# Performance work log

Hardware: AMD Instinct MI355X
Metric: run time of the kernel (lower is better)

The kernel has to match this reference:

```python
import jax, jax.numpy as jnp
import numpy as np

HEADS = 8
DIM_HEAD = 32


def setup_inputs() -> dict:
    key = jax.random.key(0)
    ks = jax.random.split(key, 10)
    B, N, D = 64, 256, 256            # B = b_true * tie_dim = 1 * 64
    INNER = HEADS * DIM_HEAD          # 256
    x = jax.random.normal(ks[0], (B, N, D), dtype=jnp.float32)
    mask = jax.random.randint(ks[1], (B, N), 0, 2).astype(bool)
    attn_bias = jax.random.normal(ks[2], (1, HEADS, N, N), dtype=jnp.float32)
    # Note: original init zeros to_out/gating weights; we use random params
    # (scaled) so the baseline output is non-trivial for correctness testing.
    s = 0.05
    Wq = jax.random.normal(ks[3], (D, INNER), dtype=jnp.float32) * s
    Wkv = jax.random.normal(ks[4], (D, 2 * INNER), dtype=jnp.float32) * s
    Wg = jax.random.normal(ks[5], (D, INNER), dtype=jnp.float32) * s
    bg = jax.random.normal(ks[6], (INNER,), dtype=jnp.float32) * s
    Wo = jax.random.normal(ks[7], (INNER, D), dtype=jnp.float32) * s
    bo = jax.random.normal(ks[8], (D,), dtype=jnp.float32) * s
    return {"x": x, "mask": mask, "attn_bias": attn_bias, "Wq": Wq,
            "Wkv": Wkv, "Wg": Wg, "bg": bg, "Wo": Wo, "bo": bo,
            "tie_dim": 64}


def reference(x, mask, attn_bias, Wq, Wkv, Wg, bg, Wo, bo, tie_dim):
    B, N, D = x.shape
    h, dh = HEADS, DIM_HEAD
    scale = dh ** -0.5

    # projections (self-attention: context = x)
    q = (x @ Wq).reshape(B, N, h, dh).transpose(0, 2, 1, 3) * scale  # b h n d
    k, v = jnp.split(x @ Wkv, 2, axis=-1)
    k = k.reshape(B, N, h, dh).transpose(0, 2, 1, 3)                 # b h n d
    v = v.reshape(B, N, h, dh).transpose(0, 2, 1, 3)                 # b h n d

    # tie_dim: average q over the r (MSA row) dim, keep per-row k
    r = tie_dim
    b = B // r
    q_tied = q.reshape(b, r, h, N, dh).mean(axis=1)                  # b h i d
    k_r = k.reshape(b, r, h, N, dh)                                  # b r h j d
    dots = jnp.einsum('bhid,brhjd->brhij', q_tied, k_r)
    dots = dots.reshape(B, h, N, N)                                  # (b r) h i j

    dots = dots + attn_bias

    # mask: pairwise row/col mask (context_mask == mask for self-attn)
    pair_mask = mask[:, None, :, None] & mask[:, None, None, :]      # B 1 i j
    mask_value = -jnp.finfo(dots.dtype).max
    dots = jnp.where(pair_mask, dots, mask_value)

    attn = jax.nn.softmax(dots, axis=-1)
    out = jnp.einsum('bhij,bhjd->bhid', attn, v)
    out = out.transpose(0, 2, 1, 3).reshape(B, N, h * dh)            # b n (h d)

    gates = jax.nn.sigmoid(x @ Wg + bg)
    out = out * gates
    return out @ Wo + bo
```

## Files before the change

### kernel.cpp

```cpp
#include <hip/hip_runtime.h>
#include <math.h>

typedef unsigned short ushort_t;
typedef unsigned int uint_t;
typedef __attribute__((ext_vector_type(8))) short short8v;
typedef __attribute__((ext_vector_type(4))) float f32x4;

#define NEG_MAX (-3.402823466e+38f)

#define OFF_KH    0
#define OFF_VP    4194304
#define OFF_GATES 6291456
#define OFF_XHI   8388608
#define OFF_ATTHI OFF_XHI
#define OFF_BTHI  12582912
#define OFF_BTLO  12713984
#define OFF_QTH   12845056
#define OFF_BIASP 12976128
#define OFF_MASK  13500416

__device__ __forceinline__ ushort_t f2bf(float x) {
    uint_t u = __float_as_uint(x);
    u = (u + 0x7fffu + ((u >> 16) & 1u)) >> 16;
    return (ushort_t)u;
}
__device__ __forceinline__ float bf2f(ushort_t u) {
    return __uint_as_float(((uint_t)u) << 16);
}
__device__ __forceinline__ void gl2lds16(const void* g, void* l) {
    typedef const __attribute__((address_space(1))) uint32_t* gptr_t;
    typedef __attribute__((address_space(3))) uint32_t* lptr_t;
    __builtin_amdgcn_global_load_lds((gptr_t)(uintptr_t)g,
                                     (lptr_t)(uintptr_t)l, 16, 0, 0);
}

__global__ __launch_bounds__(256) void prep_kernel(
    const float* __restrict__ x, const unsigned char* __restrict__ mraw,
    const float* __restrict__ bias, const float* __restrict__ Wkv,
    const float* __restrict__ Wg, const float* __restrict__ Wo,
    const float* __restrict__ Wq,
    ushort_t* __restrict__ xhi,
    uint_t* __restrict__ maskb,
    ushort_t* __restrict__ bthi, ushort_t* __restrict__ btlo,
    float* __restrict__ biasP, ushort_t* __restrict__ qPh) {
    __shared__ int cnt[256];
    __shared__ float xrow[256];
    const int bid = blockIdx.x, t = threadIdx.x;
    if (bid < 1) {
        int c = 0;
        for (int i = t; i < 4096; i += 256)
            if ((i & 3) != 0 && mraw[i] != 0) c++;
        cnt[t] = c;
        __syncthreads();
        for (int s = 128; s > 0; s >>= 1) {
            if (t < s) cnt[t] += cnt[t + s];
            __syncthreads();
        }
        int isBool = cnt[0] > 16;
        const int* mi32 = (const int*)mraw;
#pragma unroll
        for (int wq = 0; wq < 2; wq++) {
            int widx = t * 2 + wq;
            int j0 = widx * 32;
            uint_t wordv = 0;
            if (isBool) {
                for (int k = 0; k < 32; k++)
                    wordv |= (mraw[j0 + k] ? 1u : 0u) << k;
            } else {
                for (int k = 0; k < 32; k++)
                    wordv |= (mi32[j0 + k] ? 1u : 0u) << k;
            }
            maskb[widx] = wordv;
        }
    } else if (bid < 1025) {
        int idx = (bid - 1) * 256 + t;
        int n = idx >> 8, k = idx & 255;
        float v;
        if (n < 512)      v = Wkv[(size_t)k * 512 + n];
        else if (n < 768) v = Wg[(size_t)k * 256 + (n - 512)];
        else              v = Wo[(size_t)k * 256 + (n - 768)];
        ushort_t h = f2bf(v);
        bthi[idx] = h;
        btlo[idx] = f2bf(v - bf2f(h));
    } else if (bid < 1537) {
        int idx = (bid - 1025) * 256 + t;
        int lane = idx & 63, g2 = idx >> 6;
        int mf = g2 & 3, nf = (g2 >> 2) & 1, jt = (g2 >> 3) & 3;
        int iq = (g2 >> 5) & 7, h = g2 >> 8;
        int lr = lane & 15, lg = lane >> 4;
        float4 v = *(const float4*)(bias +
            (size_t)(h * 256 + iq * 32 + nf * 16 + lr) * 256 +
            jt * 64 + mf * 16 + lg * 4);
        *(float4*)(biasP + (size_t)idx * 4) = v;
    } else {
        int i = bid - 1537;
        float ssum = 0.f;
#pragma unroll 8
        for (int b8 = 0; b8 < 64; b8++) {
            size_t idx = (size_t)(b8 * 256 + i) * 256 + t;
            float v = x[idx];
            xhi[idx] = f2bf(v);
            ssum += v;
        }
        xrow[t] = ssum * (1.0f / 64.0f);
        __syncthreads();
        float s = 0.f;
        for (int k = 0; k < 256; k++)
            s = fmaf(xrow[k], Wq[(size_t)k * 256 + t], s);
        s *= 0.17677669529663687f;
        int h = t >> 5, d = t & 31, lg = d >> 3, e = d & 7;
        int g = i >> 4, lr = i & 15;
        int a = (((h * 16 + g) * 4 + lg) * 16 + lr) * 8 + e;
        qPh[a] = f2bf(s);
    }
}

template <int EPI, int MT, int NT, int TERMS>
__global__ __launch_bounds__(256) void mfma_gemm(
    const ushort_t* __restrict__ Ahi, const ushort_t* __restrict__ Alo,
    const ushort_t* __restrict__ Bthi, const ushort_t* __restrict__ Btlo,
    const float* __restrict__ bias, float* __restrict__ C,
    ushort_t* __restrict__ kh, ushort_t* __restrict__ vP,
    ushort_t* __restrict__ gatesP, int gridn) {
    constexpr int BM = MT * 32, BN = NT * 32;
    constexpr int ASZ = BM * 32 * 2;
    constexpr int BSZ = BN * 32 * 2;
    constexpr bool HAS_AL = (TERMS == 2 || TERMS == 3);
    constexpr bool HAS_BL = (TERMS == 3 || TERMS == 4);
    constexpr int AL_OFF = 2 * ASZ;
    constexpr int BH_OFF = AL_OFF + (HAS_AL ? 2 * ASZ : 0);
    constexpr int BL_OFF = BH_OFF + 2 * BSZ;
    constexpr int SMEM_BYTES = BL_OFF + (HAS_BL ? 2 * BSZ : 0);
    __shared__ __align__(16) char smem[SMEM_BYTES];
    char* aH = smem;
    char* aL = smem + AL_OFF;
    char* bH = smem + BH_OFF;
    char* bL = smem + BL_OFF;

    const int t = threadIdx.x;
    const int nwg = gridDim.x, cpx = nwg >> 3;
    const int bid = blockIdx.x;
    const int sid = (bid & 7) * cpx + (bid >> 3);
    const int m0 = (sid / gridn) * BM;
    const int n0 = (sid % gridn) * BN;
    const int wid = t >> 6, lane = t & 63;
    const int wr = wid >> 1, wc = wid & 1;
    const int lr = lane & 15, lg = lane >> 4;

    auto STAGE = [&](int d, int ks) {
        const int k0 = ks * 32;
#pragma unroll
        for (int it = 0; it < BM / 64; ++it) {
            int c = t + it * 256;
            int row = c >> 2, sub = c & 3;
            size_t ga = (size_t)(m0 + row) * 256 + k0 + sub * 8;
            gl2lds16(Ahi + ga, aH + d * ASZ + c * 16);
            if constexpr (HAS_AL)
                gl2lds16(Alo + ga, aL + d * ASZ + c * 16);
        }
#pragma unroll
        for (int it = 0; it < BN / 64; ++it) {
            int c = t + it * 256;
            int row = c >> 2, sub = c & 3;
            size_t gb = (size_t)(n0 + row) * 256 + k0 + sub * 8;
            gl2lds16(Bthi + gb, bH + d * BSZ + c * 16);
            if constexpr (HAS_BL)
                gl2lds16(Btlo + gb, bL + d * BSZ + c * 16);
        }
    };

    f32x4 acc[MT][NT] = {};

    STAGE(0, 0);
    asm volatile("s_waitcnt vmcnt(0)" ::: "memory");
    __syncthreads();

    int cur = 0;
    for (int ks = 0; ks < 8; ++ks) {
        if (ks < 7) STAGE(cur ^ 1, ks + 1);

        const ushort_t* Ap = (const ushort_t*)(aH + cur * ASZ);
        const ushort_t* ALp = (const ushort_t*)(aL + cur * ASZ);
        const ushort_t* Bp = (const ushort_t*)(bH + cur * BSZ);
        const ushort_t* BLp = (const ushort_t*)(bL + cur * BSZ);

        short8v ah[MT], al[MT], bh[NT], bl[NT];
#pragma unroll
        for (int m = 0; m < MT; m++) {
            int off = (wr * (MT * 16) + m * 16 + lr) * 32 + lg * 8;
            ah[m] = *(const short8v*)&Ap[off];
            if constexpr (HAS_AL) al[m] = *(const short8v*)&ALp[off];
        }
#pragma unroll
        for (int n = 0; n < NT; n++) {
            int off = (wc * (NT * 16) + n * 16 + lr) * 32 + lg * 8;
            bh[n] = *(const short8v*)&Bp[off];
            if constexpr (HAS_BL) bl[n] = *(const short8v*)&BLp[off];
        }
#pragma unroll
        for (int m = 0; m < MT; m++)
#pragma unroll
            for (int n = 0; n < NT; n++) {
                acc[m][n] = __builtin_amdgcn_mfma_f32_16x16x32_bf16(
                    ah[m], bh[n], acc[m][n], 0, 0, 0);
                if constexpr (HAS_AL)
                    acc[m][n] = __builtin_amdgcn_mfma_f32_16x16x32_bf16(
                        al[m], bh[n], acc[m][n], 0, 0, 0);
                if constexpr (HAS_BL)
                    acc[m][n] = __builtin_amdgcn_mfma_f32_16x16x32_bf16(
                        ah[m], bl[n], acc[m][n], 0, 0, 0);
            }

        if (ks < 7) {
            asm volatile("s_waitcnt vmcnt(0)" ::: "memory");
            __syncthreads();
        }
        cur ^= 1;
    }

#pragma unroll
    for (int m = 0; m < MT; m++)
#pragma unroll
        for (int n = 0; n < NT; n++) {
            int gr0 = m0 + wr * (MT * 16) + m * 16 + lg * 4;
            int gc = n0 + wc * (NT * 16) + n * 16 + lr;
            if (EPI == 0) {
                if (gc < 256) {
                    int hh_ = gc >> 5, dk = gc & 31;
                    int lgk = dk >> 3, ek = dk & 7;
#pragma unroll
                    for (int r = 0; r < 4; r++) {
                        int gr = gr0 + r;
                        int bb = gr >> 8, j = gr & 255;
                        int jt = j >> 6, mfk = (j >> 4) & 3, lrk = j & 15;
                        size_t a =
                            (((((size_t)(bb * 8 + hh_) * 4 + jt) * 4 + mfk) * 4
                              + lgk) * 16 + lrk) * 8 + ek;
                        kh[a] = f2bf(acc[m][n][r]);
                    }
                } else if (gc < 512) {
                    int cc = gc - 256;
                    int hh_ = cc >> 5, dv = cc & 31;
                    int mfv = dv >> 4, lrv = dv & 15;
                    int gr = gr0;
                    int bb = gr >> 8, j = gr & 255;
                    int jt = j >> 6, hbv = (j >> 5) & 1;
                    int lgv = (j >> 3) & 3, ev = j & 7;
                    size_t a =
                        ((((((size_t)(bb * 8 + hh_) * 4 + jt) * 2 + hbv) * 2
                           + mfv) * 4 + lgv) * 16 + lrv) * 8 + ev;
                    ushort4 hv;
                    hv.x = f2bf(acc[m][n][0]);
                    hv.y = f2bf(acc[m][n][1]);
                    hv.z = f2bf(acc[m][n][2]);
                    hv.w = f2bf(acc[m][n][3]);
                    *(ushort4*)(vP + a) = hv;
                } else {
                    int c = gc - 512;
                    int hh_ = c >> 5, d = c & 31;
                    int mdv = d >> 4, lga = (d >> 2) & 3, ev = d & 3;
#pragma unroll
                    for (int r = 0; r < 4; r++) {
                        int gr = gr0 + r;
                        int bb = gr >> 8, i = gr & 255;
                        int i16 = i >> 4, lra = i & 15;
                        size_t a =
                            ((((size_t)(bb * 8 + hh_) * 16 + i16) * 2 + mdv)
                             * 64 + lga * 16 + lra) * 4 + ev;
                        float v = acc[m][n][r];
                        float g = 1.f / (1.f + __expf(-(v + bias[gc - 512])));
                        gatesP[a] = f2bf(g);
                    }
                }
            } else {
#pragma unroll
                for (int r = 0; r < 4; r++)
                    C[(size_t)(gr0 + r) * 256 + gc] = acc[m][n][r] + bias[gc];
            }
        }
}

__global__ __launch_bounds__(256) void attn_mfma_kernel(
    const ushort_t* __restrict__ qPh, const ushort_t* __restrict__ kh,
    const ushort_t* __restrict__ vP, const ushort_t* __restrict__ gatesP,
    const float* __restrict__ biasP, const uint_t* __restrict__ maskb,
    ushort_t* __restrict__ atthi) {
    __shared__ __align__(16) ushort_t Pb[4][16 * 88];
    const int bid = blockIdx.x;
    const int sid = ((bid & 7) << 8) | (bid >> 3);
    const int b = sid >> 5;
    const int h = (sid >> 2) & 7;
    const int qq = sid & 3;
    const int t = threadIdx.x;
    const int w = t >> 6, lane = t & 63;
    const int lr = lane & 15, lg = lane >> 4;
    const int i0 = qq * 64 + w * 16;
    const int i16 = qq * 4 + w;
    ushort_t* pbh = Pb[w];

    uint_t mw[8];
#pragma unroll
    for (int k = 0; k < 8; k++) mw[k] = maskb[b * 8 + k];
    const uint_t mi = (mw[i0 >> 5] >> ((i0 & 31) + lr)) & 1u;

    short8v qf;
    {
        size_t off = ((((size_t)h * 16 + i16) * 4 + lg) * 16 + lr) * 8;
        qf = *(const short8v*)(qPh + off);
    }
    uint2 gva, gvb;
    {
        size_t ga = ((((size_t)(b * 8 + h) * 16 + i16) * 2 + 0) * 64 + lane) * 4;
        gva = *(const uint2*)(gatesP + ga);
        gvb = *(const uint2*)(gatesP + ga + 256);
    }

    const float* bbase = biasP +
        (size_t)(h * 256 + (i16 >> 1) * 32 + (i16 & 1) * 4) * 256 +
        (size_t)lane * 4;

    float m_run = NEG_MAX, l_run = 0.f;
    f32x4 acc_o[2] = {};

    short8v kf[2][4];
    float4 bf[2][4];
    short8v vf[2][2][2];
#pragma unroll
    for (int mf = 0; mf < 4; mf++) {
        size_t off = ((((size_t)(b * 8 + h) * 4 + 0) * 4 + mf) * 4 + lg);
        kf[0][mf] = *(const short8v*)(kh + (off * 16 + lr) * 8);
        bf[0][mf] = *(const float4*)(bbase + (size_t)mf * 256);
    }
#pragma unroll
    for (int hb = 0; hb < 2; hb++)
#pragma unroll
        for (int mv = 0; mv < 2; mv++) {
            size_t off = ((((((size_t)(b * 8 + h) * 4 + 0) * 2 + hb) * 2
                           + mv) * 4 + lg) * 16 + lr) * 8;
            vf[0][hb][mv] = *(const short8v*)(vP + off);
        }

#pragma unroll
    for (int jt = 0; jt < 4; ++jt) {
        const int cur = jt & 1, nxt = cur ^ 1;
        if (jt < 3) {
#pragma unroll
            for (int mf = 0; mf < 4; mf++) {
                size_t off = ((((size_t)(b * 8 + h) * 4 + (jt + 1)) * 4 + mf)
                              * 4 + lg);
                kf[nxt][mf] = *(const short8v*)(kh + (off * 16 + lr) * 8);
                bf[nxt][mf] = *(const float4*)(bbase +
                                               (size_t)((jt + 1) * 8 + mf) * 256);
            }
#pragma unroll
            for (int hb = 0; hb < 2; hb++)
#pragma unroll
                for (int mv = 0; mv < 2; mv++) {
                    size_t off = ((((((size_t)(b * 8 + h) * 4 + (jt + 1)) * 2
                                    + hb) * 2 + mv) * 4 + lg) * 16 + lr) * 8;
                    vf[nxt][hb][mv] = *(const short8v*)(vP + off);
                }
        }

        f32x4 s[4];
        __builtin_amdgcn_s_setprio(1);
#pragma unroll
        for (int mf = 0; mf < 4; mf++) {
            f32x4 a = {};
            s[mf] = __builtin_amdgcn_mfma_f32_16x16x32_bf16(
                kf[cur][mf], qf, a, 0, 0, 0);
        }
        __builtin_amdgcn_s_setprio(0);

#pragma unroll
        for (int mf = 0; mf < 4; mf++) {
            float4 bv = bf[cur][mf];
            uint_t bits = (mw[jt * 2 + (mf >> 1)] >> (((mf & 1) << 4) + (lg << 2)));
            s[mf][0] = ((mi & bits) & 1u)        ? s[mf][0] + bv.x : NEG_MAX;
            s[mf][1] = ((mi & (bits >> 1)) & 1u) ? s[mf][1] + bv.y : NEG_MAX;
            s[mf][2] = ((mi & (bits >> 2)) & 1u) ? s[mf][2] + bv.z : NEG_MAX;
            s[mf][3] = ((mi & (bits >> 3)) & 1u) ? s[mf][3] + bv.w : NEG_MAX;
        }

        float tm = s[0][0];
#pragma unroll
        for (int mf = 0; mf < 4; mf++)
#pragma unroll
            for (int r = 0; r < 4; r++) tm = fmaxf(tm, s[mf][r]);
        tm = fmaxf(tm, __shfl_xor(tm, 16));
        tm = fmaxf(tm, __shfl_xor(tm, 32));
        float mnew = fmaxf(m_run, tm);
        float corr = __expf(m_run - mnew);
        m_run = mnew;
#pragma unroll
        for (int md = 0; md < 2; md++)
#pragma unroll
            for (int r = 0; r < 4; r++) acc_o[md][r] *= corr;
        float ls = 0.f;
#pragma unroll
        for (int mf = 0; mf < 4; mf++)
#pragma unroll
            for (int r = 0; r < 4; r++) {
                float wv = __expf(s[mf][r] - mnew);
                s[mf][r] = wv;
                ls += wv;
            }
        ls += __shfl_xor(ls, 16);
        ls += __shfl_xor(ls, 32);
        l_run = l_run * corr + ls;

#pragma unroll
        for (int mf = 0; mf < 4; mf++) {
            uint2 hv;
            hv.x = (uint_t)f2bf(s[mf][0]) | ((uint_t)f2bf(s[mf][1]) << 16);
            hv.y = (uint_t)f2bf(s[mf][2]) | ((uint_t)f2bf(s[mf][3]) << 16);
            *(uint2*)(pbh + lr * 88 + mf * 16 + lg * 4) = hv;
        }
        asm volatile("s_waitcnt lgkmcnt(0)" ::: "memory");
        __builtin_amdgcn_sched_barrier(0);
        short8v ph0 = *(const short8v*)(pbh + lr * 88 + lg * 8);
        short8v ph1 = *(const short8v*)(pbh + lr * 88 + 32 + lg * 8);
        __builtin_amdgcn_s_setprio(1);
        acc_o[0] = __builtin_amdgcn_mfma_f32_16x16x32_bf16(
            vf[cur][0][0], ph0, acc_o[0], 0, 0, 0);
        acc_o[1] = __builtin_amdgcn_mfma_f32_16x16x32_bf16(
            vf[cur][0][1], ph0, acc_o[1], 0, 0, 0);
        acc_o[0] = __builtin_amdgcn_mfma_f32_16x16x32_bf16(
            vf[cur][1][0], ph1, acc_o[0], 0, 0, 0);
        acc_o[1] = __builtin_amdgcn_mfma_f32_16x16x32_bf16(
            vf[cur][1][1], ph1, acc_o[1], 0, 0, 0);
        __builtin_amdgcn_s_setprio(0);
    }

    float invl = 1.0f / l_run;
#pragma unroll
    for (int md = 0; md < 2; md++) {
        uint2 gv = (md == 0) ? gva : gvb;
        float g0 = bf2f((ushort_t)(gv.x & 0xffff));
        float g1 = bf2f((ushort_t)(gv.x >> 16));
        float g2 = bf2f((ushort_t)(gv.y & 0xffff));
        float g3 = bf2f((ushort_t)(gv.y >> 16));
        int i = i0 + lr;
        int d0 = md * 16 + lg * 4;
        size_t base = ((size_t)(b * 256 + i)) * 256 + h * 32 + d0;
        ushort4 hh;
        hh.x = f2bf(acc_o[md][0] * invl * g0);
        hh.y = f2bf(acc_o[md][1] * invl * g1);
        hh.z = f2bf(acc_o[md][2] * invl * g2);
        hh.w = f2bf(acc_o[md][3] * invl * g3);
        *(ushort4*)(atthi + base) = hh;
    }
}

extern "C" void kernel_launch(void* const* d_in, const int* in_sizes, int n_in,
                              void* d_out, int out_size, void* d_ws, size_t ws_size,
                              hipStream_t stream) {
    const float* x    = (const float*)d_in[0];
    const unsigned char* mraw = (const unsigned char*)d_in[1];
    const float* bias = (const float*)d_in[2];
    const float* Wq   = (const float*)d_in[3];
    const float* Wkv  = (const float*)d_in[4];
    const float* Wg   = (const float*)d_in[5];
    const float* bg   = (const float*)d_in[6];
    const float* Wo   = (const float*)d_in[7];
    const float* bo   = (const float*)d_in[8];

    float* ws = (float*)d_ws;
    ushort_t* kh     = (ushort_t*)(ws + OFF_KH);
    ushort_t* vP     = (ushort_t*)(ws + OFF_VP);
    ushort_t* gatesP = (ushort_t*)(ws + OFF_GATES);
    ushort_t* xhi    = (ushort_t*)(ws + OFF_XHI);
    ushort_t* atthi  = (ushort_t*)(ws + OFF_ATTHI);
    ushort_t* bthi   = (ushort_t*)(ws + OFF_BTHI);
    ushort_t* btlo   = (ushort_t*)(ws + OFF_BTLO);
    ushort_t* qPh    = (ushort_t*)(ws + OFF_QTH);
    float*    biasP  = ws + OFF_BIASP;
    uint_t*   maskb  = (uint_t*)(ws + OFF_MASK);

    hipLaunchKernelGGL(prep_kernel, dim3(1793), dim3(256), 0, stream,
                       x, mraw, bias, Wkv, Wg, Wo, Wq,
                       xhi, maskb, bthi, btlo, biasP, qPh);
    hipLaunchKernelGGL((mfma_gemm<0, 4, 4, 1>), dim3(768), dim3(256), 0, stream,
                       xhi, xhi, bthi, btlo, bg, (float*)nullptr,
                       kh, vP, gatesP, 6);
    hipLaunchKernelGGL(attn_mfma_kernel, dim3(2048), dim3(256), 0, stream,
                       qPh, kh, vP, gatesP, biasP, maskb, atthi);
    hipLaunchKernelGGL((mfma_gemm<1, 2, 2, 4>), dim3(1024), dim3(256), 0, stream,
                       atthi, atthi, bthi + 768 * 256, btlo + 768 * 256, bo,
                       (float*)d_out, nullptr, nullptr, nullptr, 4);
}
```

Before: 72.63 us.

## Split x row-sum across four blocks and move q projection into GEMM launch

The prep kernel's per-row mean of x over 64 MSA rows is now split across four blocks per row, which write partial sums to a new workspace buffer. The tied-q projection (mean row times Wq) moves into extra workgroups appended to the first GEMM launch, which reduce the partial sums and compute qPh. This is meant to shorten the serial tail of prep blocks that did a 64-iteration load plus a 256-long dot product, and to overlap the q projection with the KV/gates GEMM. It adds an extra global round trip for the partial sums and makes the GEMM launch heterogeneous.

```diff
diff --git a/kernel.cpp b/kernel.cpp
--- a/kernel.cpp
+++ b/kernel.cpp
@@ -18,6 +18,7 @@
 #define OFF_QTH   12845056
 #define OFF_BIASP 12976128
 #define OFF_MASK  13500416
+#define OFF_PSUM  13504512
 
 __device__ __forceinline__ ushort_t f2bf(float x) {
     uint_t u = __float_as_uint(x);
@@ -38,13 +39,11 @@
     const float* __restrict__ x, const unsigned char* __restrict__ mraw,
     const float* __restrict__ bias, const float* __restrict__ Wkv,
     const float* __restrict__ Wg, const float* __restrict__ Wo,
-    const float* __restrict__ Wq,
     ushort_t* __restrict__ xhi,
     uint_t* __restrict__ maskb,
     ushort_t* __restrict__ bthi, ushort_t* __restrict__ btlo,
-    float* __restrict__ biasP, ushort_t* __restrict__ qPh) {
+    float* __restrict__ biasP, float* __restrict__ ps) {
     __shared__ int cnt[256];
-    __shared__ float xrow[256];
     const int bid = blockIdx.x, t = threadIdx.x;
     if (bid < 1) {
         int c = 0;
@@ -93,25 +92,17 @@
             jt * 64 + mf * 16 + lg * 4);
         *(float4*)(biasP + (size_t)idx * 4) = v;
     } else {
-        int i = bid - 1537;
+        int vb2 = bid - 1537;
+        int i = vb2 >> 2, qu = vb2 & 3;
         float ssum = 0.f;
-#pragma unroll 8
-        for (int b8 = 0; b8 < 64; b8++) {
+#pragma unroll 4
+        for (int b8 = qu * 16; b8 < qu * 16 + 16; b8++) {
             size_t idx = (size_t)(b8 * 256 + i) * 256 + t;
             float v = x[idx];
             xhi[idx] = f2bf(v);
             ssum += v;
         }
-        xrow[t] = ssum * (1.0f / 64.0f);
-        __syncthreads();
-        float s = 0.f;
-        for (int k = 0; k < 256; k++)
-            s = fmaf(xrow[k], Wq[(size_t)k * 256 + t], s);
-        s *= 0.17677669529663687f;
-        int h = t >> 5, d = t & 31, lg = d >> 3, e = d & 7;
-        int g = i >> 4, lr = i & 15;
-        int a = (((h * 16 + g) * 4 + lg) * 16 + lr) * 8 + e;
-        qPh[a] = f2bf(s);
+        ps[((size_t)qu * 256 + i) * 256 + t] = ssum;
     }
 }
 
@@ -121,7 +112,9 @@
     const ushort_t* __restrict__ Bthi, const ushort_t* __restrict__ Btlo,
     const float* __restrict__ bias, float* __restrict__ C,
     ushort_t* __restrict__ kh, ushort_t* __restrict__ vP,
-    ushort_t* __restrict__ gatesP, int gridn) {
+    ushort_t* __restrict__ gatesP,
+    const float* __restrict__ Wq, const float* __restrict__ ps,
+    ushort_t* __restrict__ qPh, int nwg_gemm, int gridn) {
     constexpr int BM = MT * 32, BN = NT * 32;
     constexpr int ASZ = BM * 32 * 2;
     constexpr int BSZ = BN * 32 * 2;
@@ -138,8 +131,29 @@
     char* bL = smem + BL_OFF;
 
     const int t = threadIdx.x;
-    const int nwg = gridDim.x, cpx = nwg >> 3;
     const int bid = blockIdx.x;
+
+    if (EPI == 0 && bid >= nwg_gemm) {
+        float* xrow = (float*)smem;
+        int i = bid - nwg_gemm;
+        float s4 = ps[((size_t)0 * 256 + i) * 256 + t] +
+                   ps[((size_t)1 * 256 + i) * 256 + t] +
+                   ps[((size_t)2 * 256 + i) * 256 + t] +
+                   ps[((size_t)3 * 256 + i) * 256 + t];
+        xrow[t] = s4 * (1.0f / 64.0f);
+        __syncthreads();
+        float s = 0.f;
+        for (int k = 0; k < 256; k++)
+            s = fmaf(xrow[k], Wq[(size_t)k * 256 + t], s);
+        s *= 0.17677669529663687f;
+        int h = t >> 5, d = t & 31, lg = d >> 3, e = d & 7;
+        int g = i >> 4, lr = i & 15;
+        int a = (((h * 16 + g) * 4 + lg) * 16 + lr) * 8 + e;
+        qPh[a] = f2bf(s);
+        return;
+    }
+
+    const int cpx = nwg_gemm >> 3;
     const int sid = (bid & 7) * cpx + (bid >> 3);
     const int m0 = (sid / gridn) * BM;
     const int n0 = (sid % gridn) * BN;
@@ -476,16 +490,19 @@
     ushort_t* qPh    = (ushort_t*)(ws + OFF_QTH);
     float*    biasP  = ws + OFF_BIASP;
     uint_t*   maskb  = (uint_t*)(ws + OFF_MASK);
-
-    hipLaunchKernelGGL(prep_kernel, dim3(1793), dim3(256), 0, stream,
-                       x, mraw, bias, Wkv, Wg, Wo, Wq,
-                       xhi, maskb, bthi, btlo, biasP, qPh);
-    hipLaunchKernelGGL((mfma_gemm<0, 4, 4, 1>), dim3(768), dim3(256), 0, stream,
+    float*    ps     = ws + OFF_PSUM;
+
+    hipLaunchKernelGGL(prep_kernel, dim3(2561), dim3(256), 0, stream,
+                       x, mraw, bias, Wkv, Wg, Wo,
+                       xhi, maskb, bthi, btlo, biasP, ps);
+    hipLaunchKernelGGL((mfma_gemm<0, 4, 4, 1>), dim3(1024), dim3(256), 0, stream,
                        xhi, xhi, bthi, btlo, bg, (float*)nullptr,
-                       kh, vP, gatesP, 6);
+                       kh, vP, gatesP, Wq, ps, qPh, 768, 6);
     hipLaunchKernelGGL(attn_mfma_kernel, dim3(2048), dim3(256), 0, stream,
                        qPh, kh, vP, gatesP, biasP, maskb, atthi);
     hipLaunchKernelGGL((mfma_gemm<1, 2, 2, 4>), dim3(1024), dim3(256), 0, stream,
                        atthi, atthi, bthi + 768 * 256, btlo + 768 * 256, bo,
-                       (float*)d_out, nullptr, nullptr, nullptr, 4);
-}
+                       (float*)d_out, nullptr, nullptr, nullptr,
+                       (const float*)nullptr, (const float*)nullptr,
+                       (ushort_t*)nullptr, 1024, 4);
+}
```

Result: no change. 72.77 us (+0.2%).
